# Kernel optimization log

Hardware: AMD Instinct MI355X
Metric: run time of the kernel (lower is better)

The kernel has to match this reference:

```python
import jax, jax.numpy as jnp
import numpy as np

TOPK = 4
ROUTE_SCALE = 1.0


def setup_inputs() -> dict:
    key = jax.random.key(0)
    ks = jax.random.split(key, 16)
    B, S, C, D = 4, 512, 4, 2048
    E, H = 16, 1408
    SH = 2 * H  # n_shared_experts * moe_inter_dim
    s = 0.02
    return {
        "embeddings": jax.random.normal(ks[0], (B, S, C, D), jnp.float32),
        "x": jax.random.normal(ks[1], (B, S, C, 1), jnp.float32),
        "Wg": jax.random.normal(ks[2], (E, D), jnp.float32) * s,
        "W1": jax.random.normal(ks[3], (E, H, D), jnp.float32) * s,
        "b1": jax.random.normal(ks[4], (E, H), jnp.float32) * s,
        "W2": jax.random.normal(ks[5], (E, D, H), jnp.float32) * s,
        "b2": jax.random.normal(ks[6], (E, D), jnp.float32) * s,
        "W3": jax.random.normal(ks[7], (E, H, D), jnp.float32) * s,
        "b3": jax.random.normal(ks[8], (E, H), jnp.float32) * s,
        "Ws1": jax.random.normal(ks[9], (SH, D), jnp.float32) * s,
        "bs1": jax.random.normal(ks[10], (SH,), jnp.float32) * s,
        "Ws2": jax.random.normal(ks[11], (D, SH), jnp.float32) * s,
        "bs2": jax.random.normal(ks[12], (D,), jnp.float32) * s,
    }


def reference(embeddings, x, Wg, W1, b1, W2, b2, W3, b3, Ws1, bs1, Ws2, bs2):
    # NOTE: in the torch module, the `x` arg is immediately shadowed by
    # embeddings.view(-1, dim); it does not participate in the math.
    D = Wg.shape[1]
    E = Wg.shape[0]
    xt = embeddings.reshape(-1, D)  # [N, D] flattened tokens

    # Gate: softmax scores (fp32), top-k routing; n_groups == 1, no gate bias.
    logits = jnp.einsum("nd,ed->ne", xt, Wg)
    scores = jax.nn.softmax(logits.astype(jnp.float32), axis=-1)  # [N, E]
    topv, idx = jax.lax.top_k(scores, TOPK)  # values == gathered original scores
    weights = (topv * ROUTE_SCALE).astype(xt.dtype)  # [N, K]

    # Expert dispatch/combine. Per-token combined weight for expert e is
    # sum_k weights[n, k] * (idx[n, k] == e); unassigned tokens get weight 0,
    # so masked-dense per-expert SwiGLU reproduces the gather/scatter math.
    y = jnp.zeros_like(xt)
    for e in range(E):
        w_e = jnp.sum(weights * (idx == e).astype(weights.dtype), axis=1)  # [N]
        h = jax.nn.silu(xt @ W1[e].T + b1[e]) * (xt @ W3[e].T + b3[e])  # [N, H]
        y = y + (h @ W2[e].T + b2[e]) * w_e[:, None]

    # Shared experts: Linear -> SiLU -> Linear applied to every token.
    z = jax.nn.silu(xt @ Ws1.T + bs1) @ Ws2.T + bs2

    return (y + z).reshape(embeddings.shape)
```

## Files before the change

kernel.cpp:

```cpp
#include <hip/hip_runtime.h>
#include <stdint.h>

#define N_TOK 8192
#define DIM   2048
#define NEXP  16
#define HID   1408
#define SHID  2816
#define KTOP  4
#define TILEMAX 272

typedef __attribute__((ext_vector_type(8))) short bf16x8;
typedef __attribute__((ext_vector_type(4))) float f32x4;

#define MFMA16(a,b,c) __builtin_amdgcn_mfma_f32_16x16x32_bf16((a),(b),(c),0,0,0)

__device__ __forceinline__ unsigned short f2b(float f){
  unsigned u = __float_as_uint(f);
  return (unsigned short)((u + 0x7fffu + ((u >> 16) & 1u)) >> 16);
}
__device__ __forceinline__ unsigned pk2(float a, float b){
  return (unsigned)f2b(a) | ((unsigned)f2b(b) << 16);
}
__device__ __forceinline__ float bu2f(unsigned hs){ return __uint_as_float(hs << 16); }
__device__ __forceinline__ float siluf(float x){ return x / (1.f + expf(-x)); }
__device__ __forceinline__ f32x4 zero4(){ f32x4 z; z[0]=0.f; z[1]=0.f; z[2]=0.f; z[3]=0.f; return z; }

__device__ __forceinline__ void gll16(const unsigned short* g, unsigned short* l){
  __builtin_amdgcn_global_load_lds(
      (const __attribute__((address_space(1))) void*)g,
      (__attribute__((address_space(3))) void*)l, 16, 0, 0);
}

#define SEGW ((size_t)NEXP*HID*DIM/4)
#define SEGS ((size_t)SHID*DIM/4)
__global__ __launch_bounds__(256) void k_cvtW(const float* __restrict__ W1, const float* __restrict__ W3,
                                              const float* __restrict__ W2, const float* __restrict__ Ws1,
                                              const float* __restrict__ Ws2,
                                              unsigned short* __restrict__ d1, unsigned short* __restrict__ d3,
                                              unsigned short* __restrict__ d2, unsigned short* __restrict__ ds1,
                                              unsigned short* __restrict__ ds2){
  size_t total = 3*SEGW + 2*SEGS;
  for (size_t i = (size_t)blockIdx.x*256 + threadIdx.x; i < total; i += (size_t)gridDim.x*256){
    const float* s; unsigned short* d; size_t off;
    if      (i <   SEGW)        { s = W1;  d = d1;  off = i; }
    else if (i < 2*SEGW)        { s = W3;  d = d3;  off = i - SEGW; }
    else if (i < 3*SEGW)        { s = W2;  d = d2;  off = i - 2*SEGW; }
    else if (i < 3*SEGW + SEGS) { s = Ws1; d = ds1; off = i - 3*SEGW; }
    else                        { s = Ws2; d = ds2; off = i - 3*SEGW - SEGS; }
    float4 v = ((const float4*)s)[off];
    uint2 q; q.x = pk2(v.x, v.y); q.y = pk2(v.z, v.w);
    ((uint2*)d)[off] = q;
  }
}

__global__ __launch_bounds__(256) void k_gate(const float* __restrict__ X, const float* __restrict__ Wg,
                                              float* __restrict__ topw, int* __restrict__ topi,
                                              int* __restrict__ cnt, unsigned short* __restrict__ Xb){
  int lane = threadIdx.x & 63;
  int t = blockIdx.x*4 + (threadIdx.x >> 6);
  const float* xr = X + (size_t)t*DIM;
  float4 xv[8];
#pragma unroll
  for (int i=0;i<8;i++){
    xv[i] = *(const float4*)(xr + i*256 + lane*4);
    uint2 q; q.x = pk2(xv[i].x, xv[i].y); q.y = pk2(xv[i].z, xv[i].w);
    *(uint2*)(Xb + (size_t)t*DIM + i*256 + lane*4) = q;
  }
  float sc[NEXP];
#pragma unroll
  for (int e=0;e<NEXP;e++){
    const float* wr = Wg + e*DIM;
    float s = 0.f;
#pragma unroll
    for (int i=0;i<8;i++){
      float4 w = *(const float4*)(wr + i*256 + lane*4);
      s = fmaf(xv[i].x, w.x, s); s = fmaf(xv[i].y, w.y, s);
      s = fmaf(xv[i].z, w.z, s); s = fmaf(xv[i].w, w.w, s);
    }
#pragma unroll
    for (int d=1; d<64; d<<=1) s += __shfl_xor(s, d);
    sc[e] = s;
  }
  if (lane == 0){
    float m = sc[0];
#pragma unroll
    for (int e=1;e<NEXP;e++) m = fmaxf(m, sc[e]);
    float den = 0.f;
#pragma unroll
    for (int e=0;e<NEXP;e++){ sc[e] = expf(sc[e]-m); den += sc[e]; }
    float inv = 1.f/den;
#pragma unroll
    for (int e=0;e<NEXP;e++) sc[e] *= inv;
    for (int k=0;k<KTOP;k++){
      int bi = 0; float bv = sc[0];
#pragma unroll
      for (int e=1;e<NEXP;e++) if (sc[e] > bv){ bv = sc[e]; bi = e; }
      topw[t*KTOP+k] = bv;
      topi[t*KTOP+k] = bi;
#pragma unroll
      for (int e=0;e<NEXP;e++) if (e == bi) sc[e] = -1.f;
      atomicAdd(&cnt[bi], 1);
    }
  }
}

__global__ void k_scan(const int* __restrict__ cnt, int* __restrict__ off, int* __restrict__ cur,
                       int* __restrict__ tab){
  if (threadIdx.x == 0){
    int a = 0;
    for (int e=0;e<NEXP;e++){ off[e] = a; cur[e] = a; a += cnt[e]; }
    int n = 0;
    for (int e=0;e<NEXP;e++){
      int nt = (cnt[e] + 127) >> 7;
      for (int r=0;r<nt;r++) tab[n++] = (e << 16) | r;
    }
    for (; n < TILEMAX; ++n) tab[n] = -1;
  }
}

__global__ __launch_bounds__(256) void k_place(const int* __restrict__ topi, const float* __restrict__ topw,
                                               int* __restrict__ cur, int* __restrict__ rows,
                                               float* __restrict__ rw, int* __restrict__ slotL){
  int t = blockIdx.x*256 + threadIdx.x;
#pragma unroll
  for (int k=0;k<KTOP;k++){
    int e = topi[t*KTOP+k];
    int p = atomicAdd(&cur[e], 1);
    rows[p] = t;
    rw[p]   = topw[t*KTOP+k];
    slotL[t*KTOP+k] = p;
  }
}

template<int ROUNDS>
__device__ __forceinline__ void stage_Bf(unsigned short* lsB, const float* bF,
                                         int ldK, int bn0, int k0, int tid){
#pragma unroll
  for (int j=0;j<ROUNDS;j++){
    int idx = j*256 + tid, r = idx >> 4, c4 = idx & 15;
    float4 v = *(const float4*)(bF + (size_t)(bn0 + r)*ldK + k0 + c4*4);
    uint2 q; q.x = pk2(v.x, v.y); q.y = pk2(v.z, v.w);
    *(uint2*)&lsB[r*64 + (((c4 >> 1) ^ (r & 7)) << 3) + ((c4 & 1) << 2)] = q;
  }
}

__device__ __forceinline__ void read_A(bf16x8 af[4], const unsigned short* lsA, int wm, int lane, int kc){
  int s = kc*4 + (lane >> 4);
#pragma unroll
  for (int mi=0;mi<4;mi++){
    int r = wm + mi*16 + (lane & 15);
    af[mi] = *(const bf16x8*)&lsA[r*64 + ((s ^ (r & 7)) << 3)];
  }
}

template<bool WBF>
__global__ __launch_bounds__(256,2) void k_g13(const unsigned short* __restrict__ Xb,
    const void* __restrict__ W1p, const void* __restrict__ W3p,
    const float* __restrict__ b1, const float* __restrict__ b3,
    const int* __restrict__ rows, const int* __restrict__ cnt, const int* __restrict__ offs,
    const int* __restrict__ tab, unsigned short* __restrict__ H1)
{
  int bid = blockIdx.x;
  int l = bid >> 3;
  int ct = l / 34;
  int slot = (bid & 7)*34 + (l - ct*34);
  int ent = tab[slot];
  if (ent < 0) return;
  int e = ent >> 16, rt = ent & 0xffff;
  int cntE = cnt[e];
  int offE = offs[e];
  int hn0 = ct*128;
  int tid = threadIdx.x, lane = tid & 63, wid = tid >> 6;
  int wm = (wid >> 1)*64, wn = (wid & 1)*64;
  __shared__ alignas(16) unsigned short lsA[8192], lsB1[8192], lsB3[8192];

  int lr8 = lane >> 3;
  int cx  = (lane & 7) ^ lr8;
  unsigned offA[4];
#pragma unroll
  for (int j=0;j<4;j++){
    int lrow = rt*128 + wid*32 + j*8 + lr8;
    int arow = rows[offE + (lrow < cntE ? lrow : cntE-1)];
    offA[j] = (unsigned)arow*DIM + (unsigned)cx*8;
  }
  unsigned offB0 = (unsigned)(hn0 + wid*32 + lr8)*DIM + (unsigned)cx*8;
  const unsigned short* b1H = (const unsigned short*)W1p + (size_t)e*HID*DIM;
  const unsigned short* b3H = (const unsigned short*)W3p + (size_t)e*HID*DIM;
  const float* b1F = (const float*)W1p + (size_t)e*HID*DIM;
  const float* b3F = (const float*)W3p + (size_t)e*HID*DIM;
  unsigned short* lA  = &lsA[wid*2048];
  unsigned short* lB1 = &lsB1[wid*2048];
  unsigned short* lB3 = &lsB3[wid*2048];

  f32x4 acc1[4][4], acc3[4][4];
#pragma unroll
  for (int i=0;i<4;i++)
#pragma unroll
    for (int j=0;j<4;j++){ acc1[i][j] = zero4(); acc3[i][j] = zero4(); }

  for (int kt=0; kt<DIM/64; ++kt){
    int k0 = kt*64;
    __syncthreads();
#pragma unroll
    for (int j=0;j<4;j++){
      gll16(Xb + offA[j] + k0, lA + j*512);
      if constexpr (WBF){
        gll16(b1H + offB0 + j*(8*DIM) + k0, lB1 + j*512);
        gll16(b3H + offB0 + j*(8*DIM) + k0, lB3 + j*512);
      }
    }
    if constexpr (!WBF){
      stage_Bf<8>(lsB1, b1F, DIM, hn0, k0, tid);
      stage_Bf<8>(lsB3, b3F, DIM, hn0, k0, tid);
    }
    __syncthreads();
#pragma unroll
    for (int kc=0;kc<2;kc++){
      bf16x8 af[4]; read_A(af, lsA, wm, lane, kc);
      int sB = kc*4 + (lane >> 4);
#pragma unroll
      for (int nj=0;nj<4;nj++){
        int rb = wn + nj*16 + (lane & 15);
        int lof = rb*64 + ((sB ^ (rb & 7)) << 3);
        bf16x8 bf1 = *(const bf16x8*)&lsB1[lof];
        bf16x8 bf3 = *(const bf16x8*)&lsB3[lof];
#pragma unroll
        for (int mi=0;mi<4;mi++){
          acc1[mi][nj] = MFMA16(af[mi], bf1, acc1[mi][nj]);
          acc3[mi][nj] = MFMA16(af[mi], bf3, acc3[mi][nj]);
        }
      }
    }
  }
#pragma unroll
  for (int nj=0;nj<4;nj++){
    int h = hn0 + wn + nj*16 + (lane & 15);
    float b1v = b1[e*HID + h];
    float b3v = b3[e*HID + h];
#pragma unroll
    for (int mi=0;mi<4;mi++){
#pragma unroll
      for (int r=0;r<4;r++){
        int gr = rt*128 + wm + mi*16 + (lane >> 4)*4 + r;
        if (gr < cntE){
          float u = acc1[mi][nj][r] + b1v;
          float v = acc3[mi][nj][r] + b3v;
          H1[(size_t)(offE + gr)*HID + h] = f2b(siluf(u)*v);
        }
      }
    }
  }
}

template<int MODE, bool WBF, int KSTEPS>
__global__ __launch_bounds__(256,2) void k_gemm(const unsigned short* __restrict__ Abase,
    const void* __restrict__ Bpv, const float* __restrict__ bias,
    float* __restrict__ outF, unsigned short* __restrict__ outH,
    const int* __restrict__ rows, const float* __restrict__ rw,
    const int* __restrict__ cnt, const int* __restrict__ offs,
    const int* __restrict__ tab)
{
  constexpr int KD = KSTEPS*64;
  int e = 0, ct, rt, cntE = 0, offE = 0;
  int bid = blockIdx.x;
  int l = bid >> 3;
  if constexpr (MODE >= 2){
    ct = l / 34;
    int slot = (bid & 7)*34 + (l - ct*34);
    int ent = tab[slot];
    if (ent < 0) return;
    e = ent >> 16; rt = ent & 0xffff;
    cntE = cnt[e];
    offE = offs[e];
  } else {
    rt = (bid & 7)*8 + (l & 7);
    ct = l >> 3;
  }
  int bn0 = ct*256, t0 = rt*128;
  int tid = threadIdx.x, lane = tid & 63, wid = tid >> 6;
  int wm = (wid >> 1)*64, wn = (wid & 1)*128;
  __shared__ alignas(16) unsigned short lsA[8192], lsB[16384];

  int lr8 = lane >> 3;
  int cx  = (lane & 7) ^ lr8;
  unsigned offA0 = 0;
  unsigned offA[4];
  if constexpr (MODE >= 2){
#pragma unroll
    for (int j=0;j<4;j++){
      int lrow = t0 + wid*32 + j*8 + lr8;
      int arow = offE + (lrow < cntE ? lrow : cntE-1);
      offA[j] = (unsigned)arow*KD + (unsigned)cx*8;
    }
  } else {
    offA0 = (unsigned)(t0 + wid*32 + lr8)*KD + (unsigned)cx*8;
  }
  unsigned offB0 = (unsigned)(bn0 + wid*64 + lr8)*KD + (unsigned)cx*8;
  const unsigned short* bH = (const unsigned short*)Bpv + ((MODE >= 2) ? (size_t)e*2048*KD : (size_t)0);
  const float*          bF = (const float*)Bpv          + ((MODE >= 2) ? (size_t)e*2048*KD : (size_t)0);
  const float* biasp = bias + ((MODE >= 2) ? e*DIM : 0);
  unsigned short* lA = &lsA[wid*2048];
  unsigned short* lB = &lsB[wid*4096];

  f32x4 acc[4][8];
#pragma unroll
  for (int i=0;i<4;i++)
#pragma unroll
    for (int j=0;j<8;j++) acc[i][j] = zero4();

  for (int kt=0; kt<KSTEPS; ++kt){
    int k0 = kt*64;
    __syncthreads();
#pragma unroll
    for (int j=0;j<4;j++){
      if constexpr (MODE >= 2) gll16(Abase + offA[j] + k0, lA + j*512);
      else                     gll16(Abase + offA0 + j*(8*KD) + k0, lA + j*512);
    }
    if constexpr (WBF){
#pragma unroll
      for (int j=0;j<8;j++) gll16(bH + offB0 + j*(8*KD) + k0, lB + j*512);
    } else {
      stage_Bf<16>(lsB, bF, KD, bn0, k0, tid);
    }
    __syncthreads();
#pragma unroll
    for (int kc=0;kc<2;kc++){
      bf16x8 af[4]; read_A(af, lsA, wm, lane, kc);
      int sB = kc*4 + (lane >> 4);
#pragma unroll
      for (int nj=0;nj<8;nj++){
        int rb = wn + nj*16 + (lane & 15);
        bf16x8 bfr = *(const bf16x8*)&lsB[rb*64 + ((sB ^ (rb & 7)) << 3)];
#pragma unroll
        for (int mi=0;mi<4;mi++)
          acc[mi][nj] = MFMA16(af[mi], bfr, acc[mi][nj]);
      }
    }
  }
#pragma unroll
  for (int nj=0;nj<8;nj++){
    int col = bn0 + wn + nj*16 + (lane & 15);
    float bv = biasp[col];
#pragma unroll
    for (int mi=0;mi<4;mi++){
#pragma unroll
      for (int r=0;r<4;r++){
        int lr = wm + mi*16 + (lane >> 4)*4 + r;
        float v = acc[mi][nj][r] + bv;
        if constexpr (MODE == 0){
          outH[(size_t)(t0 + lr)*SHID + col] = f2b(siluf(v));
        } else if constexpr (MODE == 1){
          outF[(size_t)(t0 + lr)*DIM + col] = v;
        } else {
          int gr = t0 + lr;
          if (gr < cntE){
            int slot = offE + gr;
            float wv = rw[slot] * v;
            if constexpr (MODE == 2){
              atomicAdd(outF + (size_t)rows[slot]*DIM + col, wv);
            } else {
              outH[(size_t)slot*DIM + col] = f2b(wv);
            }
          }
        }
      }
    }
  }
}

__global__ __launch_bounds__(256) void k_comb(const unsigned short* __restrict__ Yr,
                                              const int* __restrict__ slotL, float* __restrict__ out){
  int i = blockIdx.x*256 + threadIdx.x;
  int t = i >> 8, c = i & 255;
  size_t ob = (size_t)t*DIM + (size_t)c*8;
  float4 a = *(float4*)(out + ob);
  float4 b = *(float4*)(out + ob + 4);
  int sl[4];
#pragma unroll
  for (int k=0;k<KTOP;k++) sl[k] = slotL[t*KTOP + k];
#pragma unroll
  for (int k=0;k<KTOP;k++){
    uint4 v = *(const uint4*)(Yr + (size_t)sl[k]*DIM + (size_t)c*8);
    a.x += bu2f(v.x & 0xffffu); a.y += bu2f(v.x >> 16);
    a.z += bu2f(v.y & 0xffffu); a.w += bu2f(v.y >> 16);
    b.x += bu2f(v.z & 0xffffu); b.y += bu2f(v.z >> 16);
    b.z += bu2f(v.w & 0xffffu); b.w += bu2f(v.w >> 16);
  }
  *(float4*)(out + ob) = a;
  *(float4*)(out + ob + 4) = b;
}

extern "C" void kernel_launch(void* const* d_in, const int* in_sizes, int n_in,
                              void* d_out, int out_size, void* d_ws, size_t ws_size,
                              hipStream_t stream)
{
  (void)in_sizes; (void)n_in; (void)out_size;
  const float* emb = (const float*)d_in[0];
  const float* Wg  = (const float*)d_in[2];
  const float* W1  = (const float*)d_in[3];
  const float* b1  = (const float*)d_in[4];
  const float* W2  = (const float*)d_in[5];
  const float* b2  = (const float*)d_in[6];
  const float* W3  = (const float*)d_in[7];
  const float* b3  = (const float*)d_in[8];
  const float* Ws1 = (const float*)d_in[9];
  const float* bs1 = (const float*)d_in[10];
  const float* Ws2 = (const float*)d_in[11];
  const float* bs2 = (const float*)d_in[12];
  float* out = (float*)d_out;
  char* ws = (char*)d_ws;

  const size_t SZ_XB = (size_t)N_TOK*DIM*2;
  const size_t SZ_H1 = (size_t)N_TOK*KTOP*HID*2;
  const size_t SZ_HS = (size_t)N_TOK*SHID*2;
  const size_t SZ_T4 = (size_t)N_TOK*KTOP*4;
  const size_t SZ_WB = (size_t)NEXP*HID*DIM*2;
  const size_t SZ_SB = (size_t)SHID*DIM*2;
  const size_t SZ_YR = (size_t)N_TOK*KTOP*DIM*2;

  size_t off_xb = 0;
  size_t off_h1 = off_xb + SZ_XB;
  size_t off_hs = off_h1 + SZ_H1;
  size_t off_tw = off_hs + SZ_HS;
  size_t off_ti = off_tw + SZ_T4;
  size_t off_ro = off_ti + SZ_T4;
  size_t off_rw = off_ro + SZ_T4;
  size_t off_sl = off_rw + SZ_T4;
  size_t off_cnt = off_sl + SZ_T4;
  size_t off_off = off_cnt + 256;
  size_t off_cur = off_off + 256;
  size_t off_tab = off_cur + 256;
  size_t base_end = off_tab + TILEMAX*4 + 64;
  size_t off_w1b = base_end;
  size_t off_w3b = off_w1b + SZ_WB;
  size_t off_w2b = off_w3b + SZ_WB;
  size_t off_s1b = off_w2b + SZ_WB;
  size_t off_s2b = off_s1b + SZ_SB;
  size_t wbf_end = off_s2b + SZ_SB;

  bool wbf = ws_size >= wbf_end;
  size_t off_yr = wbf ? wbf_end : base_end;
  bool comb = ws_size >= off_yr + SZ_YR;

  unsigned short* Xb = (unsigned short*)(ws + off_xb);
  unsigned short* H1 = (unsigned short*)(ws + off_h1);
  unsigned short* Hs = (unsigned short*)(ws + off_hs);
  float* topw = (float*)(ws + off_tw);
  int*   topi = (int*)(ws + off_ti);
  int*   rowsL= (int*)(ws + off_ro);
  float* rwL  = (float*)(ws + off_rw);
  int*   slotL= (int*)(ws + off_sl);
  int*   cntP = (int*)(ws + off_cnt);
  int*   offP = (int*)(ws + off_off);
  int*   curP = (int*)(ws + off_cur);
  int*   tabP = (int*)(ws + off_tab);
  unsigned short* Yr = (unsigned short*)(ws + off_yr);

  hipMemsetAsync(ws + off_cnt, 0, 768, stream);
  if (wbf){
    k_cvtW<<<4096, 256, 0, stream>>>(W1, W3, W2, Ws1, Ws2,
        (unsigned short*)(ws + off_w1b), (unsigned short*)(ws + off_w3b),
        (unsigned short*)(ws + off_w2b), (unsigned short*)(ws + off_s1b),
        (unsigned short*)(ws + off_s2b));
  }
  k_gate<<<2048, 256, 0, stream>>>(emb, Wg, topw, topi, cntP, Xb);
  k_scan<<<1, 64, 0, stream>>>(cntP, offP, curP, tabP);
  k_place<<<32, 256, 0, stream>>>(topi, topw, curP, rowsL, rwL, slotL);

  if (wbf) k_g13<true ><<<2992, 256, 0, stream>>>(Xb, ws+off_w1b, ws+off_w3b, b1, b3, rowsL, cntP, offP, tabP, H1);
  else     k_g13<false><<<2992, 256, 0, stream>>>(Xb, W1, W3, b1, b3, rowsL, cntP, offP, tabP, H1);

  if (wbf) k_gemm<0,true ,32><<<704, 256, 0, stream>>>(Xb, ws+off_s1b, bs1, nullptr, Hs, nullptr,nullptr,nullptr,nullptr,nullptr);
  else     k_gemm<0,false,32><<<704, 256, 0, stream>>>(Xb, Ws1, bs1, nullptr, Hs, nullptr,nullptr,nullptr,nullptr,nullptr);

  if (wbf) k_gemm<1,true ,44><<<512, 256, 0, stream>>>(Hs, ws+off_s2b, bs2, out, nullptr, nullptr,nullptr,nullptr,nullptr,nullptr);
  else     k_gemm<1,false,44><<<512, 256, 0, stream>>>(Hs, Ws2, bs2, out, nullptr, nullptr,nullptr,nullptr,nullptr,nullptr);

  if (comb){
    if (wbf) k_gemm<3,true ,22><<<2176, 256, 0, stream>>>(H1, ws+off_w2b, b2, nullptr, Yr, rowsL, rwL, cntP, offP, tabP);
    else     k_gemm<3,false,22><<<2176, 256, 0, stream>>>(H1, W2, b2, nullptr, Yr, rowsL, rwL, cntP, offP, tabP);
    k_comb<<<N_TOK, 256, 0, stream>>>(Yr, slotL, out);
  } else {
    if (wbf) k_gemm<2,true ,22><<<2176, 256, 0, stream>>>(H1, ws+off_w2b, b2, out, nullptr, rowsL, rwL, cntP, offP, tabP);
    else     k_gemm<2,false,22><<<2176, 256, 0, stream>>>(H1, W2, b2, out, nullptr, rowsL, rwL, cntP, offP, tabP);
  }
}
```

Baseline: 1.839 ms.

## Retile MoE GEMMs to 256-row tiles with 512-thread, 8-wave blocks

All grouped and shared GEMM kernels move from 256-thread blocks with 128-row tiles to 512-thread blocks with 256-row token tiles. The gate/up kernel keeps 128 hidden columns per tile, while the down-projection and shared GEMMs shrink to 128 output columns. The expert tile table is rebuilt for 256-row tiles and the global-to-LDS load indexing is rewritten for the new thread layout. The aim is more weight reuse per loaded tile and fewer per-block overheads. In exchange, tiles grow by up to 255 padded rows per expert and the gate/up kernel needs more LDS per block, which may limit occupancy.

```diff
diff --git a/kernel.cpp b/kernel.cpp
--- a/kernel.cpp
+++ b/kernel.cpp
@@ -7,7 +7,7 @@
 #define HID   1408
 #define SHID  2816
 #define KTOP  4
-#define TILEMAX 272
+#define TILEMAX 144
 
 typedef __attribute__((ext_vector_type(8))) short bf16x8;
 typedef __attribute__((ext_vector_type(4))) float f32x4;
@@ -111,7 +111,7 @@
     for (int e=0;e<NEXP;e++){ off[e] = a; cur[e] = a; a += cnt[e]; }
     int n = 0;
     for (int e=0;e<NEXP;e++){
-      int nt = (cnt[e] + 127) >> 7;
+      int nt = (cnt[e] + 255) >> 8;
       for (int r=0;r<nt;r++) tab[n++] = (e << 16) | r;
     }
     for (; n < TILEMAX; ++n) tab[n] = -1;
@@ -132,12 +132,11 @@
   }
 }
 
-template<int ROUNDS>
-__device__ __forceinline__ void stage_Bf(unsigned short* lsB, const float* bF,
-                                         int ldK, int bn0, int k0, int tid){
-#pragma unroll
-  for (int j=0;j<ROUNDS;j++){
-    int idx = j*256 + tid, r = idx >> 4, c4 = idx & 15;
+__device__ __forceinline__ void stage_Bf512(unsigned short* lsB, const float* bF,
+                                            int ldK, int bn0, int k0, int tid){
+#pragma unroll
+  for (int j=0;j<4;j++){
+    int idx = j*512 + tid, r = idx >> 4, c4 = idx & 15;
     float4 v = *(const float4*)(bF + (size_t)(bn0 + r)*ldK + k0 + c4*4);
     uint2 q; q.x = pk2(v.x, v.y); q.y = pk2(v.z, v.w);
     *(uint2*)&lsB[r*64 + (((c4 >> 1) ^ (r & 7)) << 3) + ((c4 & 1) << 2)] = q;
@@ -154,7 +153,7 @@
 }
 
 template<bool WBF>
-__global__ __launch_bounds__(256,2) void k_g13(const unsigned short* __restrict__ Xb,
+__global__ __launch_bounds__(512,2) void k_g13(const unsigned short* __restrict__ Xb,
     const void* __restrict__ W1p, const void* __restrict__ W3p,
     const float* __restrict__ b1, const float* __restrict__ b3,
     const int* __restrict__ rows, const int* __restrict__ cnt, const int* __restrict__ offs,
@@ -162,8 +161,8 @@
 {
   int bid = blockIdx.x;
   int l = bid >> 3;
-  int ct = l / 34;
-  int slot = (bid & 7)*34 + (l - ct*34);
+  int ct = l / 18;
+  int slot = (bid & 7)*18 + (l - ct*18);
   int ent = tab[slot];
   if (ent < 0) return;
   int e = ent >> 16, rt = ent & 0xffff;
@@ -172,25 +171,23 @@
   int hn0 = ct*128;
   int tid = threadIdx.x, lane = tid & 63, wid = tid >> 6;
   int wm = (wid >> 1)*64, wn = (wid & 1)*64;
-  __shared__ alignas(16) unsigned short lsA[8192], lsB1[8192], lsB3[8192];
-
-  int lr8 = lane >> 3;
-  int cx  = (lane & 7) ^ lr8;
+  __shared__ alignas(16) unsigned short lsA[16384], lsB1[8192], lsB3[8192];
+
+  int r0 = tid >> 3;
+  int cx = (tid & 7) ^ (r0 & 7);
   unsigned offA[4];
 #pragma unroll
   for (int j=0;j<4;j++){
-    int lrow = rt*128 + wid*32 + j*8 + lr8;
+    int lrow = rt*256 + j*64 + r0;
     int arow = rows[offE + (lrow < cntE ? lrow : cntE-1)];
     offA[j] = (unsigned)arow*DIM + (unsigned)cx*8;
   }
-  unsigned offB0 = (unsigned)(hn0 + wid*32 + lr8)*DIM + (unsigned)cx*8;
+  unsigned offB0 = (unsigned)(hn0 + r0)*DIM + (unsigned)cx*8;
   const unsigned short* b1H = (const unsigned short*)W1p + (size_t)e*HID*DIM;
   const unsigned short* b3H = (const unsigned short*)W3p + (size_t)e*HID*DIM;
   const float* b1F = (const float*)W1p + (size_t)e*HID*DIM;
   const float* b3F = (const float*)W3p + (size_t)e*HID*DIM;
-  unsigned short* lA  = &lsA[wid*2048];
-  unsigned short* lB1 = &lsB1[wid*2048];
-  unsigned short* lB3 = &lsB3[wid*2048];
+  unsigned dst0 = (unsigned)tid*8;
 
   f32x4 acc1[4][4], acc3[4][4];
 #pragma unroll
@@ -202,16 +199,16 @@
     int k0 = kt*64;
     __syncthreads();
 #pragma unroll
-    for (int j=0;j<4;j++){
-      gll16(Xb + offA[j] + k0, lA + j*512);
-      if constexpr (WBF){
-        gll16(b1H + offB0 + j*(8*DIM) + k0, lB1 + j*512);
-        gll16(b3H + offB0 + j*(8*DIM) + k0, lB3 + j*512);
+    for (int j=0;j<4;j++) gll16(Xb + offA[j] + k0, &lsA[dst0 + j*4096]);
+    if constexpr (WBF){
+#pragma unroll
+      for (int j=0;j<2;j++){
+        gll16(b1H + offB0 + j*(64*DIM) + k0, &lsB1[dst0 + j*4096]);
+        gll16(b3H + offB0 + j*(64*DIM) + k0, &lsB3[dst0 + j*4096]);
       }
-    }
-    if constexpr (!WBF){
-      stage_Bf<8>(lsB1, b1F, DIM, hn0, k0, tid);
-      stage_Bf<8>(lsB3, b3F, DIM, hn0, k0, tid);
+    } else {
+      stage_Bf512(lsB1, b1F, DIM, hn0, k0, tid);
+      stage_Bf512(lsB3, b3F, DIM, hn0, k0, tid);
     }
     __syncthreads();
 #pragma unroll
@@ -241,7 +238,7 @@
     for (int mi=0;mi<4;mi++){
 #pragma unroll
       for (int r=0;r<4;r++){
-        int gr = rt*128 + wm + mi*16 + (lane >> 4)*4 + r;
+        int gr = rt*256 + wm + mi*16 + (lane >> 4)*4 + r;
         if (gr < cntE){
           float u = acc1[mi][nj][r] + b1v;
           float v = acc3[mi][nj][r] + b3v;
@@ -253,7 +250,7 @@
 }
 
 template<int MODE, bool WBF, int KSTEPS>
-__global__ __launch_bounds__(256,2) void k_gemm(const unsigned short* __restrict__ Abase,
+__global__ __launch_bounds__(512,2) void k_gemm(const unsigned short* __restrict__ Abase,
     const void* __restrict__ Bpv, const float* __restrict__ bias,
     float* __restrict__ outF, unsigned short* __restrict__ outH,
     const int* __restrict__ rows, const float* __restrict__ rw,
@@ -265,62 +262,55 @@
   int bid = blockIdx.x;
   int l = bid >> 3;
   if constexpr (MODE >= 2){
-    ct = l / 34;
-    int slot = (bid & 7)*34 + (l - ct*34);
+    ct = l / 18;
+    int slot = (bid & 7)*18 + (l - ct*18);
     int ent = tab[slot];
     if (ent < 0) return;
     e = ent >> 16; rt = ent & 0xffff;
     cntE = cnt[e];
     offE = offs[e];
   } else {
-    rt = (bid & 7)*8 + (l & 7);
-    ct = l >> 3;
-  }
-  int bn0 = ct*256, t0 = rt*128;
+    rt = (bid & 7)*4 + (l & 3);
+    ct = l >> 2;
+  }
+  int bn0 = ct*128, t0 = rt*256;
   int tid = threadIdx.x, lane = tid & 63, wid = tid >> 6;
-  int wm = (wid >> 1)*64, wn = (wid & 1)*128;
-  __shared__ alignas(16) unsigned short lsA[8192], lsB[16384];
-
-  int lr8 = lane >> 3;
-  int cx  = (lane & 7) ^ lr8;
-  unsigned offA0 = 0;
+  int wm = (wid >> 1)*64, wn = (wid & 1)*64;
+  __shared__ alignas(16) unsigned short lsA[16384], lsB[8192];
+
+  int r0 = tid >> 3;
+  int cx = (tid & 7) ^ (r0 & 7);
   unsigned offA[4];
-  if constexpr (MODE >= 2){
-#pragma unroll
-    for (int j=0;j<4;j++){
-      int lrow = t0 + wid*32 + j*8 + lr8;
-      int arow = offE + (lrow < cntE ? lrow : cntE-1);
-      offA[j] = (unsigned)arow*KD + (unsigned)cx*8;
-    }
-  } else {
-    offA0 = (unsigned)(t0 + wid*32 + lr8)*KD + (unsigned)cx*8;
-  }
-  unsigned offB0 = (unsigned)(bn0 + wid*64 + lr8)*KD + (unsigned)cx*8;
+#pragma unroll
+  for (int j=0;j<4;j++){
+    int lrow = t0 + j*64 + r0;
+    int arow;
+    if constexpr (MODE >= 2) arow = offE + (lrow < cntE ? lrow : cntE-1);
+    else                     arow = lrow;
+    offA[j] = (unsigned)arow*KD + (unsigned)cx*8;
+  }
+  unsigned offB0 = (unsigned)(bn0 + r0)*KD + (unsigned)cx*8;
   const unsigned short* bH = (const unsigned short*)Bpv + ((MODE >= 2) ? (size_t)e*2048*KD : (size_t)0);
   const float*          bF = (const float*)Bpv          + ((MODE >= 2) ? (size_t)e*2048*KD : (size_t)0);
   const float* biasp = bias + ((MODE >= 2) ? e*DIM : 0);
-  unsigned short* lA = &lsA[wid*2048];
-  unsigned short* lB = &lsB[wid*4096];
-
-  f32x4 acc[4][8];
+  unsigned dst0 = (unsigned)tid*8;
+
+  f32x4 acc[4][4];
 #pragma unroll
   for (int i=0;i<4;i++)
 #pragma unroll
-    for (int j=0;j<8;j++) acc[i][j] = zero4();
+    for (int j=0;j<4;j++) acc[i][j] = zero4();
 
   for (int kt=0; kt<KSTEPS; ++kt){
     int k0 = kt*64;
     __syncthreads();
 #pragma unroll
-    for (int j=0;j<4;j++){
-      if constexpr (MODE >= 2) gll16(Abase + offA[j] + k0, lA + j*512);
-      else                     gll16(Abase + offA0 + j*(8*KD) + k0, lA + j*512);
-    }
+    for (int j=0;j<4;j++) gll16(Abase + offA[j] + k0, &lsA[dst0 + j*4096]);
     if constexpr (WBF){
 #pragma unroll
-      for (int j=0;j<8;j++) gll16(bH + offB0 + j*(8*KD) + k0, lB + j*512);
+      for (int j=0;j<2;j++) gll16(bH + offB0 + j*(64*KD) + k0, &lsB[dst0 + j*4096]);
     } else {
-      stage_Bf<16>(lsB, bF, KD, bn0, k0, tid);
+      stage_Bf512(lsB, bF, KD, bn0, k0, tid);
     }
     __syncthreads();
 #pragma unroll
@@ -328,7 +318,7 @@
       bf16x8 af[4]; read_A(af, lsA, wm, lane, kc);
       int sB = kc*4 + (lane >> 4);
 #pragma unroll
-      for (int nj=0;nj<8;nj++){
+      for (int nj=0;nj<4;nj++){
         int rb = wn + nj*16 + (lane & 15);
         bf16x8 bfr = *(const bf16x8*)&lsB[rb*64 + ((sB ^ (rb & 7)) << 3)];
 #pragma unroll
@@ -338,7 +328,7 @@
     }
   }
 #pragma unroll
-  for (int nj=0;nj<8;nj++){
+  for (int nj=0;nj<4;nj++){
     int col = bn0 + wn + nj*16 + (lane & 15);
     float bv = biasp[col];
 #pragma unroll
@@ -467,21 +457,21 @@
   k_scan<<<1, 64, 0, stream>>>(cntP, offP, curP, tabP);
   k_place<<<32, 256, 0, stream>>>(topi, topw, curP, rowsL, rwL, slotL);
 
-  if (wbf) k_g13<true ><<<2992, 256, 0, stream>>>(Xb, ws+off_w1b, ws+off_w3b, b1, b3, rowsL, cntP, offP, tabP, H1);
-  else     k_g13<false><<<2992, 256, 0, stream>>>(Xb, W1, W3, b1, b3, rowsL, cntP, offP, tabP, H1);
-
-  if (wbf) k_gemm<0,true ,32><<<704, 256, 0, stream>>>(Xb, ws+off_s1b, bs1, nullptr, Hs, nullptr,nullptr,nullptr,nullptr,nullptr);
-  else     k_gemm<0,false,32><<<704, 256, 0, stream>>>(Xb, Ws1, bs1, nullptr, Hs, nullptr,nullptr,nullptr,nullptr,nullptr);
-
-  if (wbf) k_gemm<1,true ,44><<<512, 256, 0, stream>>>(Hs, ws+off_s2b, bs2, out, nullptr, nullptr,nullptr,nullptr,nullptr,nullptr);
-  else     k_gemm<1,false,44><<<512, 256, 0, stream>>>(Hs, Ws2, bs2, out, nullptr, nullptr,nullptr,nullptr,nullptr,nullptr);
+  if (wbf) k_g13<true ><<<1584, 512, 0, stream>>>(Xb, ws+off_w1b, ws+off_w3b, b1, b3, rowsL, cntP, offP, tabP, H1);
+  else     k_g13<false><<<1584, 512, 0, stream>>>(Xb, W1, W3, b1, b3, rowsL, cntP, offP, tabP, H1);
+
+  if (wbf) k_gemm<0,true ,32><<<704, 512, 0, stream>>>(Xb, ws+off_s1b, bs1, nullptr, Hs, nullptr,nullptr,nullptr,nullptr,nullptr);
+  else     k_gemm<0,false,32><<<704, 512, 0, stream>>>(Xb, Ws1, bs1, nullptr, Hs, nullptr,nullptr,nullptr,nullptr,nullptr);
+
+  if (wbf) k_gemm<1,true ,44><<<512, 512, 0, stream>>>(Hs, ws+off_s2b, bs2, out, nullptr, nullptr,nullptr,nullptr,nullptr,nullptr);
+  else     k_gemm<1,false,44><<<512, 512, 0, stream>>>(Hs, Ws2, bs2, out, nullptr, nullptr,nullptr,nullptr,nullptr,nullptr);
 
   if (comb){
-    if (wbf) k_gemm<3,true ,22><<<2176, 256, 0, stream>>>(H1, ws+off_w2b, b2, nullptr, Yr, rowsL, rwL, cntP, offP, tabP);
-    else     k_gemm<3,false,22><<<2176, 256, 0, stream>>>(H1, W2, b2, nullptr, Yr, rowsL, rwL, cntP, offP, tabP);
+    if (wbf) k_gemm<3,true ,22><<<2304, 512, 0, stream>>>(H1, ws+off_w2b, b2, nullptr, Yr, rowsL, rwL, cntP, offP, tabP);
+    else     k_gemm<3,false,22><<<2304, 512, 0, stream>>>(H1, W2, b2, nullptr, Yr, rowsL, rwL, cntP, offP, tabP);
     k_comb<<<N_TOK, 256, 0, stream>>>(Yr, slotL, out);
   } else {
-    if (wbf) k_gemm<2,true ,22><<<2176, 256, 0, stream>>>(H1, ws+off_w2b, b2, out, nullptr, rowsL, rwL, cntP, offP, tabP);
-    else     k_gemm<2,false,22><<<2176, 256, 0, stream>>>(H1, W2, b2, out, nullptr, rowsL, rwL, cntP, offP, tabP);
-  }
-}
+    if (wbf) k_gemm<2,true ,22><<<2304, 512, 0, stream>>>(H1, ws+off_w2b, b2, out, nullptr, rowsL, rwL, cntP, offP, tabP);
+    else     k_gemm<2,false,22><<<2304, 512, 0, stream>>>(H1, W2, b2, out, nullptr, rowsL, rwL, cntP, offP, tabP);
+  }
+}
```

After: 1.811 ms. Within noise of the previous version (-1.5%).

## Halve GEMM N-tile to 128 and fuse expert combine into shared-expert output GEMM

Applied to the files above, without the earlier changes.

Shrinks the generic GEMM tile from 128x256 to 128x128 (fewer accumulators, smaller B LDS buffer, doubled grid sizes), which should raise occupancy and wave count. Removes the separate k_comb kernel by adding a MODE 4 epilogue to the shared-expert second GEMM that gathers the four routed bf16 expert outputs per token and adds them before the single write to out. It also reorders launches so the routed W2 GEMM runs before the shared path. The cost is more B reloads per A tile, and the gathers in the epilogue are scalar and uncoalesced.

```diff
diff --git a/kernel.cpp b/kernel.cpp
--- a/kernel.cpp
+++ b/kernel.cpp
@@ -132,11 +132,10 @@
   }
 }
 
-template<int ROUNDS>
 __device__ __forceinline__ void stage_Bf(unsigned short* lsB, const float* bF,
                                          int ldK, int bn0, int k0, int tid){
 #pragma unroll
-  for (int j=0;j<ROUNDS;j++){
+  for (int j=0;j<8;j++){
     int idx = j*256 + tid, r = idx >> 4, c4 = idx & 15;
     float4 v = *(const float4*)(bF + (size_t)(bn0 + r)*ldK + k0 + c4*4);
     uint2 q; q.x = pk2(v.x, v.y); q.y = pk2(v.z, v.w);
@@ -210,8 +209,8 @@
       }
     }
     if constexpr (!WBF){
-      stage_Bf<8>(lsB1, b1F, DIM, hn0, k0, tid);
-      stage_Bf<8>(lsB3, b3F, DIM, hn0, k0, tid);
+      stage_Bf(lsB1, b1F, DIM, hn0, k0, tid);
+      stage_Bf(lsB3, b3F, DIM, hn0, k0, tid);
     }
     __syncthreads();
 #pragma unroll
@@ -258,13 +257,15 @@
     float* __restrict__ outF, unsigned short* __restrict__ outH,
     const int* __restrict__ rows, const float* __restrict__ rw,
     const int* __restrict__ cnt, const int* __restrict__ offs,
-    const int* __restrict__ tab)
+    const int* __restrict__ tab,
+    const unsigned short* __restrict__ YrIn, const int* __restrict__ slotL4)
 {
+  constexpr bool EXPERT = (MODE == 2 || MODE == 3);
   constexpr int KD = KSTEPS*64;
   int e = 0, ct, rt, cntE = 0, offE = 0;
   int bid = blockIdx.x;
   int l = bid >> 3;
-  if constexpr (MODE >= 2){
+  if constexpr (EXPERT){
     ct = l / 34;
     int slot = (bid & 7)*34 + (l - ct*34);
     int ent = tab[slot];
@@ -276,16 +277,16 @@
     rt = (bid & 7)*8 + (l & 7);
     ct = l >> 3;
   }
-  int bn0 = ct*256, t0 = rt*128;
+  int bn0 = ct*128, t0 = rt*128;
   int tid = threadIdx.x, lane = tid & 63, wid = tid >> 6;
-  int wm = (wid >> 1)*64, wn = (wid & 1)*128;
-  __shared__ alignas(16) unsigned short lsA[8192], lsB[16384];
+  int wm = (wid >> 1)*64, wn = (wid & 1)*64;
+  __shared__ alignas(16) unsigned short lsA[8192], lsB[8192];
 
   int lr8 = lane >> 3;
   int cx  = (lane & 7) ^ lr8;
   unsigned offA0 = 0;
   unsigned offA[4];
-  if constexpr (MODE >= 2){
+  if constexpr (EXPERT){
 #pragma unroll
     for (int j=0;j<4;j++){
       int lrow = t0 + wid*32 + j*8 + lr8;
@@ -295,40 +296,36 @@
   } else {
     offA0 = (unsigned)(t0 + wid*32 + lr8)*KD + (unsigned)cx*8;
   }
-  unsigned offB0 = (unsigned)(bn0 + wid*64 + lr8)*KD + (unsigned)cx*8;
-  const unsigned short* bH = (const unsigned short*)Bpv + ((MODE >= 2) ? (size_t)e*2048*KD : (size_t)0);
-  const float*          bF = (const float*)Bpv          + ((MODE >= 2) ? (size_t)e*2048*KD : (size_t)0);
-  const float* biasp = bias + ((MODE >= 2) ? e*DIM : 0);
+  unsigned offB0 = (unsigned)(bn0 + wid*32 + lr8)*KD + (unsigned)cx*8;
+  const unsigned short* bH = (const unsigned short*)Bpv + (EXPERT ? (size_t)e*2048*KD : (size_t)0);
+  const float*          bF = (const float*)Bpv          + (EXPERT ? (size_t)e*2048*KD : (size_t)0);
+  const float* biasp = bias + (EXPERT ? e*DIM : 0);
   unsigned short* lA = &lsA[wid*2048];
-  unsigned short* lB = &lsB[wid*4096];
-
-  f32x4 acc[4][8];
+  unsigned short* lB = &lsB[wid*2048];
+
+  f32x4 acc[4][4];
 #pragma unroll
   for (int i=0;i<4;i++)
 #pragma unroll
-    for (int j=0;j<8;j++) acc[i][j] = zero4();
+    for (int j=0;j<4;j++) acc[i][j] = zero4();
 
   for (int kt=0; kt<KSTEPS; ++kt){
     int k0 = kt*64;
     __syncthreads();
 #pragma unroll
     for (int j=0;j<4;j++){
-      if constexpr (MODE >= 2) gll16(Abase + offA[j] + k0, lA + j*512);
-      else                     gll16(Abase + offA0 + j*(8*KD) + k0, lA + j*512);
-    }
-    if constexpr (WBF){
-#pragma unroll
-      for (int j=0;j<8;j++) gll16(bH + offB0 + j*(8*KD) + k0, lB + j*512);
-    } else {
-      stage_Bf<16>(lsB, bF, KD, bn0, k0, tid);
-    }
+      if constexpr (EXPERT) gll16(Abase + offA[j] + k0, lA + j*512);
+      else                  gll16(Abase + offA0 + j*(8*KD) + k0, lA + j*512);
+      if constexpr (WBF)    gll16(bH + offB0 + j*(8*KD) + k0, lB + j*512);
+    }
+    if constexpr (!WBF) stage_Bf(lsB, bF, KD, bn0, k0, tid);
     __syncthreads();
 #pragma unroll
     for (int kc=0;kc<2;kc++){
       bf16x8 af[4]; read_A(af, lsA, wm, lane, kc);
       int sB = kc*4 + (lane >> 4);
 #pragma unroll
-      for (int nj=0;nj<8;nj++){
+      for (int nj=0;nj<4;nj++){
         int rb = wn + nj*16 + (lane & 15);
         bf16x8 bfr = *(const bf16x8*)&lsB[rb*64 + ((sB ^ (rb & 7)) << 3)];
 #pragma unroll
@@ -338,7 +335,7 @@
     }
   }
 #pragma unroll
-  for (int nj=0;nj<8;nj++){
+  for (int nj=0;nj<4;nj++){
     int col = bn0 + wn + nj*16 + (lane & 15);
     float bv = biasp[col];
 #pragma unroll
@@ -351,6 +348,15 @@
           outH[(size_t)(t0 + lr)*SHID + col] = f2b(siluf(v));
         } else if constexpr (MODE == 1){
           outF[(size_t)(t0 + lr)*DIM + col] = v;
+        } else if constexpr (MODE == 4){
+          int t = t0 + lr;
+          float s = v;
+#pragma unroll
+          for (int k=0;k<KTOP;k++){
+            int sl2 = slotL4[t*KTOP + k];
+            s += bu2f(YrIn[(size_t)sl2*DIM + col]);
+          }
+          outF[(size_t)t*DIM + col] = s;
         } else {
           int gr = t0 + lr;
           if (gr < cntE){
@@ -366,28 +372,6 @@
       }
     }
   }
-}
-
-__global__ __launch_bounds__(256) void k_comb(const unsigned short* __restrict__ Yr,
-                                              const int* __restrict__ slotL, float* __restrict__ out){
-  int i = blockIdx.x*256 + threadIdx.x;
-  int t = i >> 8, c = i & 255;
-  size_t ob = (size_t)t*DIM + (size_t)c*8;
-  float4 a = *(float4*)(out + ob);
-  float4 b = *(float4*)(out + ob + 4);
-  int sl[4];
-#pragma unroll
-  for (int k=0;k<KTOP;k++) sl[k] = slotL[t*KTOP + k];
-#pragma unroll
-  for (int k=0;k<KTOP;k++){
-    uint4 v = *(const uint4*)(Yr + (size_t)sl[k]*DIM + (size_t)c*8);
-    a.x += bu2f(v.x & 0xffffu); a.y += bu2f(v.x >> 16);
-    a.z += bu2f(v.y & 0xffffu); a.w += bu2f(v.y >> 16);
-    b.x += bu2f(v.z & 0xffffu); b.y += bu2f(v.z >> 16);
-    b.z += bu2f(v.w & 0xffffu); b.w += bu2f(v.w >> 16);
-  }
-  *(float4*)(out + ob) = a;
-  *(float4*)(out + ob + 4) = b;
 }
 
 extern "C" void kernel_launch(void* const* d_in, const int* in_sizes, int n_in,
@@ -470,18 +454,19 @@
   if (wbf) k_g13<true ><<<2992, 256, 0, stream>>>(Xb, ws+off_w1b, ws+off_w3b, b1, b3, rowsL, cntP, offP, tabP, H1);
   else     k_g13<false><<<2992, 256, 0, stream>>>(Xb, W1, W3, b1, b3, rowsL, cntP, offP, tabP, H1);
 
-  if (wbf) k_gemm<0,true ,32><<<704, 256, 0, stream>>>(Xb, ws+off_s1b, bs1, nullptr, Hs, nullptr,nullptr,nullptr,nullptr,nullptr);
-  else     k_gemm<0,false,32><<<704, 256, 0, stream>>>(Xb, Ws1, bs1, nullptr, Hs, nullptr,nullptr,nullptr,nullptr,nullptr);
-
-  if (wbf) k_gemm<1,true ,44><<<512, 256, 0, stream>>>(Hs, ws+off_s2b, bs2, out, nullptr, nullptr,nullptr,nullptr,nullptr,nullptr);
-  else     k_gemm<1,false,44><<<512, 256, 0, stream>>>(Hs, Ws2, bs2, out, nullptr, nullptr,nullptr,nullptr,nullptr,nullptr);
-
   if (comb){
-    if (wbf) k_gemm<3,true ,22><<<2176, 256, 0, stream>>>(H1, ws+off_w2b, b2, nullptr, Yr, rowsL, rwL, cntP, offP, tabP);
-    else     k_gemm<3,false,22><<<2176, 256, 0, stream>>>(H1, W2, b2, nullptr, Yr, rowsL, rwL, cntP, offP, tabP);
-    k_comb<<<N_TOK, 256, 0, stream>>>(Yr, slotL, out);
+    if (wbf) k_gemm<3,true ,22><<<4352, 256, 0, stream>>>(H1, ws+off_w2b, b2, nullptr, Yr, rowsL, rwL, cntP, offP, tabP, nullptr, nullptr);
+    else     k_gemm<3,false,22><<<4352, 256, 0, stream>>>(H1, W2, b2, nullptr, Yr, rowsL, rwL, cntP, offP, tabP, nullptr, nullptr);
+    if (wbf) k_gemm<0,true ,32><<<1408, 256, 0, stream>>>(Xb, ws+off_s1b, bs1, nullptr, Hs, nullptr,nullptr,nullptr,nullptr,nullptr, nullptr, nullptr);
+    else     k_gemm<0,false,32><<<1408, 256, 0, stream>>>(Xb, Ws1, bs1, nullptr, Hs, nullptr,nullptr,nullptr,nullptr,nullptr, nullptr, nullptr);
+    if (wbf) k_gemm<4,true ,44><<<1024, 256, 0, stream>>>(Hs, ws+off_s2b, bs2, out, nullptr, nullptr,nullptr,nullptr,nullptr,nullptr, Yr, slotL);
+    else     k_gemm<4,false,44><<<1024, 256, 0, stream>>>(Hs, Ws2, bs2, out, nullptr, nullptr,nullptr,nullptr,nullptr,nullptr, Yr, slotL);
   } else {
-    if (wbf) k_gemm<2,true ,22><<<2176, 256, 0, stream>>>(H1, ws+off_w2b, b2, out, nullptr, rowsL, rwL, cntP, offP, tabP);
-    else     k_gemm<2,false,22><<<2176, 256, 0, stream>>>(H1, W2, b2, out, nullptr, rowsL, rwL, cntP, offP, tabP);
-  }
-}
+    if (wbf) k_gemm<0,true ,32><<<1408, 256, 0, stream>>>(Xb, ws+off_s1b, bs1, nullptr, Hs, nullptr,nullptr,nullptr,nullptr,nullptr, nullptr, nullptr);
+    else     k_gemm<0,false,32><<<1408, 256, 0, stream>>>(Xb, Ws1, bs1, nullptr, Hs, nullptr,nullptr,nullptr,nullptr,nullptr, nullptr, nullptr);
+    if (wbf) k_gemm<1,true ,44><<<1024, 256, 0, stream>>>(Hs, ws+off_s2b, bs2, out, nullptr, nullptr,nullptr,nullptr,nullptr,nullptr, nullptr, nullptr);
+    else     k_gemm<1,false,44><<<1024, 256, 0, stream>>>(Hs, Ws2, bs2, out, nullptr, nullptr,nullptr,nullptr,nullptr,nullptr, nullptr, nullptr);
+    if (wbf) k_gemm<2,true ,22><<<4352, 256, 0, stream>>>(H1, ws+off_w2b, b2, out, nullptr, rowsL, rwL, cntP, offP, tabP, nullptr, nullptr);
+    else     k_gemm<2,false,22><<<4352, 256, 0, stream>>>(H1, W2, b2, out, nullptr, rowsL, rwL, cntP, offP, tabP, nullptr, nullptr);
+  }
+}
```

Measured after the change: 1.911 ms. 3.9% more time.
